# Performance work log

Hardware: AMD Instinct MI355X
Metric: run time of the kernel (lower is better)

## Reference

```python
import jax, jax.numpy as jnp
import numpy as np


def _lstm_dir(x, w_ih, w_hh, b_ih, b_hh, reverse):
    # x: [B, L, D]; w_ih: [4H, D]; w_hh: [4H, H]; PyTorch gate order i,f,g,o
    B = x.shape[0]
    H = w_hh.shape[1]
    h0 = jnp.zeros((B, H), x.dtype)

    def cell(carry, x_t):
        h, c = carry
        z = x_t @ w_ih.T + h @ w_hh.T + b_ih + b_hh
        i, f, g, o = jnp.split(z, 4, axis=-1)
        c = jax.nn.sigmoid(f) * c + jax.nn.sigmoid(i) * jnp.tanh(g)
        h = jax.nn.sigmoid(o) * jnp.tanh(c)
        return (h, c), h

    _, hs = jax.lax.scan(cell, (h0, h0), jnp.swapaxes(x, 0, 1), reverse=reverse)
    return jnp.swapaxes(hs, 0, 1)  # [B, L, H]


def setup_inputs() -> dict:
    key = jax.random.key(0)
    ks = jax.random.split(key, 16)
    B, L, V, D, H, E, A = 32, 128, 30000, 300, 128, 34, 36
    s = 0.05
    rn = lambda k, shape: jax.random.normal(k, shape, jnp.float32) * s
    return {
        "input_ids": jax.random.randint(ks[0], (B, L), 0, V),
        "emb": rn(ks[1], (V, D)),
        "w_ih_f": rn(ks[2], (4 * H, D)), "w_hh_f": rn(ks[3], (4 * H, H)),
        "b_ih_f": rn(ks[4], (4 * H,)), "b_hh_f": rn(ks[5], (4 * H,)),
        "w_ih_b": rn(ks[6], (4 * H, D)), "w_hh_b": rn(ks[7], (4 * H, H)),
        "b_ih_b": rn(ks[8], (4 * H,)), "b_hh_b": rn(ks[9], (4 * H,)),
        "event_w": rn(ks[10], (E, 2 * H)), "event_b": rn(ks[11], (E,)),
        "arg_w": rn(ks[12], (A, 4 * H + E - 1)), "arg_b": rn(ks[13], (A,)),
    }


def reference(input_ids, emb, w_ih_f, w_hh_f, b_ih_f, b_hh_f,
              w_ih_b, w_hh_b, b_ih_b, b_hh_b,
              event_w, event_b, arg_w, arg_b):
    # Eval mode: dropout is identity. No labels -> return (event_logits, arguments_logits).
    B, L = input_ids.shape
    E = event_b.shape[0]
    x = emb[input_ids]  # [B, L, D]
    h_f = _lstm_dir(x, w_ih_f, w_hh_f, b_ih_f, b_hh_f, False)
    h_b = _lstm_dir(x, w_ih_b, w_hh_b, b_ih_b, b_hh_b, True)
    hidden = jnp.concatenate([h_f, h_b], axis=-1)  # [B, L, 2H]
    col_range = jnp.arange(E - 1)
    g0 = jnp.zeros((B, L, E - 1), hidden.dtype)  # running g_trg_arg memory

    def step(g, h_i):  # h_i: [B, 2H] = trigger hidden state at timestep i
        ev_logit = h_i @ event_w.T + event_b  # [B, E]
        ev_pred = jnp.argmax(ev_logit, axis=-1)  # [B]
        trig = jnp.broadcast_to(h_i[:, None, :], hidden.shape)  # [B, L, 2H]
        ah = jnp.concatenate([hidden, trig, g], axis=-1)  # [B, L, 4H+E-1]
        arg_logit = ah @ arg_w.T + arg_b  # [B, L, A]
        arg_pred = jnp.argmax(arg_logit, axis=-1)  # [B, L]
        # Vectorized update_g_trg_arg: for batch items with ev_pred>0, set
        # column (ev_pred-1) to 1 wherever arg_pred>0, else keep previous value.
        mask_ev = ev_pred > 0  # [B]
        col = jnp.where(mask_ev, ev_pred - 1, 0)  # [B]
        onehot = (col[:, None] == col_range[None, :]) & mask_ev[:, None]  # [B, E-1]
        cond = onehot[:, None, :] & (arg_pred[:, :, None] > 0)  # [B, L, E-1]
        g = jnp.where(cond, jnp.ones((), g.dtype), g)
        return g, (ev_logit, arg_logit)

    _, (ev_logits, arg_logits) = jax.lax.scan(step, g0, jnp.swapaxes(hidden, 0, 1))
    event_logits = jnp.swapaxes(ev_logits, 0, 1)  # [B, L, E]
    arguments_logits = jnp.swapaxes(arg_logits, 0, 1)  # [B, L, L, A]
    return event_logits, arguments_logits
```

## Files before the change

kernel.cpp:

```cpp
#include <hip/hip_runtime.h>
#include <hip/hip_bf16.h>
#include <stdint.h>

#define B_  32
#define L_  128
#define D_  300
#define DP_ 304
#define H_  128
#define G_  512
#define E_  34
#define A_  36
#define M_  4096
#define NC_ 106
#define NCP 112
#define CH_ 8
#define NCH 16
#define LCH 8
#define NCHK (L_ / LCH)

__device__ __forceinline__ float sigf(float x){ return 1.0f / (1.0f + expf(-x)); }

__global__ void k_prep1(const float* __restrict__ wihf, const float* __restrict__ wihb,
                        float* __restrict__ WT){
    int k = blockIdx.x;
    int d = blockIdx.y;
    int n = threadIdx.x;
    const float* w = d ? wihb : wihf;
    WT[((size_t)d * DP_ + k) * G_ + n] = (k < D_) ? w[(size_t)n * D_ + k] : 0.0f;
}

__global__ void k_prep2(const float* __restrict__ evw, const float* __restrict__ evb,
                        const float* __restrict__ argw, const float* __restrict__ argb,
                        float* __restrict__ WcatT, float* __restrict__ biasv){
    int k = blockIdx.x;
    int n = threadIdx.x;
    if (n >= NCP) return;
    float v = 0.0f;
    if (n < E_)       v = evw[(size_t)n * 256 + k];
    else if (n < 70)  v = argw[(size_t)(n - 34) * 545 + k];
    else if (n < NC_) v = argw[(size_t)(n - 70) * 545 + 256 + k];
    WcatT[(size_t)k * NCP + n] = v;
    if (k == 0){
        float bv = 0.0f;
        if (n < E_) bv = evb[n];
        else if (n < 70) bv = argb[n - 34];
        biasv[n] = bv;
    }
}

__launch_bounds__(256)
__global__ void k_gemm1(const int* __restrict__ ids, const float* __restrict__ emb,
                        const float* __restrict__ WT,
                        const float* __restrict__ bihf, const float* __restrict__ bhhf,
                        const float* __restrict__ bihb, const float* __restrict__ bhhb,
                        float* __restrict__ XW){
    __shared__ __align__(16) float xs[DP_][8];
    int d  = blockIdx.y;
    int m0 = blockIdx.x * 8;
    int tid = threadIdx.x;
    for (int idx = tid; idx < 8 * DP_; idx += 256){
        int r = idx / DP_, k = idx % DP_;
        int id = ids[m0 + r];
        xs[k][r] = (k < D_) ? emb[(size_t)id * D_ + k] : 0.0f;
    }
    __syncthreads();
    int n0 = tid, n1 = tid + 256;
    const float* w0 = WT + (size_t)d * DP_ * G_ + n0;
    const float* w1 = WT + (size_t)d * DP_ * G_ + n1;
    const float4* xs4 = (const float4*)xs;
    float acc0[8] = {}, acc1[8] = {};
    #pragma unroll 2
    for (int k = 0; k < D_; k++){
        float wv0 = w0[(size_t)k * G_];
        float wv1 = w1[(size_t)k * G_];
        float4 xA = xs4[k * 2], xB = xs4[k * 2 + 1];
        acc0[0] += xA.x * wv0; acc0[1] += xA.y * wv0;
        acc0[2] += xA.z * wv0; acc0[3] += xA.w * wv0;
        acc0[4] += xB.x * wv0; acc0[5] += xB.y * wv0;
        acc0[6] += xB.z * wv0; acc0[7] += xB.w * wv0;
        acc1[0] += xA.x * wv1; acc1[1] += xA.y * wv1;
        acc1[2] += xA.z * wv1; acc1[3] += xA.w * wv1;
        acc1[4] += xB.x * wv1; acc1[5] += xB.y * wv1;
        acc1[6] += xB.z * wv1; acc1[7] += xB.w * wv1;
    }
    float bias0 = d ? (bihb[n0] + bhhb[n0]) : (bihf[n0] + bhhf[n0]);
    float bias1 = d ? (bihb[n1] + bhhb[n1]) : (bihf[n1] + bhhf[n1]);
    for (int r = 0; r < 8; r++){
        XW[((size_t)d * M_ + m0 + r) * G_ + n0] = acc0[r] + bias0;
        XW[((size_t)d * M_ + m0 + r) * G_ + n1] = acc1[r] + bias1;
    }
}

#define PF(XR, CHI)                                                             \
{                                                                               \
    if ((CHI) < NCHK){                                                          \
        _Pragma("unroll")                                                       \
        for (int j = 0; j < LCH; j++){                                          \
            int s_ = (CHI) * LCH + j;                                           \
            int t_ = d ? (L_ - 1 - s_) : s_;                                    \
            XR[j] = xwn[(size_t)t_ * G_];                                       \
        }                                                                       \
    }                                                                           \
}

#define STEP8(XR, CHI)                                                          \
{                                                                               \
    _Pragma("unroll")                                                           \
    for (int j = 0; j < LCH; j++){                                              \
        int s_ = (CHI) * LCH + j;                                               \
        const float4* hc = (const float4*)((j & 1) ? hb1 : hb0);                \
        float a0=0.f,a1=0.f,a2=0.f,a3=0.f;                                      \
        _Pragma("unroll")                                                       \
        for (int q = 0; q < 32; q++){                                           \
            float4 hv = hc[q];                                                  \
            a0 += wv[q].x * hv.x; a1 += wv[q].y * hv.y;                         \
            a2 += wv[q].z * hv.z; a3 += wv[q].w * hv.w;                         \
        }                                                                       \
        float z = XR[j] + ((a0 + a1) + (a2 + a3));                              \
        float v = (gi == 2) ? tanhf(z) : sigf(z);                               \
        float Fv = __shfl_xor(v, 16);                                           \
        float Gv = __shfl_xor(v, 32);                                           \
        float Ov = __shfl_xor(v, 48);                                           \
        if (lane < 16){                                                         \
            c = Fv * c + v * Gv;                                                \
            float h = Ov * tanhf(c);                                            \
            float* hw = (j & 1) ? hb0 : hb1;                                    \
            hw[n16] = h;                                                        \
            hist[(size_t)(s_) * H_ + n16] = h;                                  \
        }                                                                       \
        __syncthreads();                                                        \
    }                                                                           \
}

__launch_bounds__(512, 2)
__global__ void k_lstm(const float* __restrict__ XW, const float* __restrict__ whhf,
                       const float* __restrict__ whhb, float* __restrict__ Hid){
    __shared__ __align__(16) float hb0[H_];
    __shared__ __align__(16) float hb1[H_];
    __shared__ __align__(16) float hist[L_ * H_];
    int bid = blockIdx.x;
    int d = bid >> 5, b = bid & 31;
    int tid = threadIdx.x;
    int wvi  = tid >> 6;
    int lane = tid & 63;
    int n16  = wvi * 16 + (lane & 15);
    int gi   = lane >> 4;
    int row  = gi * H_ + n16;
    const float* whh = d ? whhb : whhf;
    const float4* wr = (const float4*)(whh + (size_t)row * H_);
    float4 wv[32];
    #pragma unroll
    for (int q = 0; q < 32; q++) wv[q] = wr[q];
    float c = 0.0f;
    if (tid < H_) hb0[tid] = 0.0f;
    __syncthreads();
    const float* xwn = XW + ((size_t)d * M_ + (size_t)b * L_) * G_ + row;
    float xA[LCH], xB[LCH];
    PF(xA, 0)
    #pragma unroll 1
    for (int cp = 0; cp < NCHK / 2; cp++){
        PF(xB, 2 * cp + 1)
        STEP8(xA, 2 * cp)
        PF(xA, 2 * cp + 2)
        STEP8(xB, 2 * cp + 1)
    }
    const float4* hist4 = (const float4*)hist;
    #pragma unroll
    for (int q = 0; q < 8; q++){
        int idx = tid + q * 512;
        int sl = idx >> 5, n4 = idx & 31;
        int t_ = d ? (L_ - 1 - sl) : sl;
        *(float4*)(Hid + ((size_t)b * L_ + t_) * 256 + d * H_ + n4 * 4) =
            hist4[(size_t)sl * 32 + n4];
    }
}

__launch_bounds__(128)
__global__ void k_heads2(const float* __restrict__ Hid, const float* __restrict__ WcatT,
                         const float* __restrict__ biasv,
                         float* __restrict__ out0, float* __restrict__ Base,
                         float* __restrict__ T2, int* __restrict__ Evcol){
    __shared__ float hs[256];
    __shared__ float evl[E_];
    int m = blockIdx.x;
    int tid = threadIdx.x;
    hs[tid]       = Hid[(size_t)m * 256 + tid];
    hs[tid + 128] = Hid[(size_t)m * 256 + 128 + tid];
    __syncthreads();
    float acc = 0.0f;
    if (tid < NC_){
        const float* wc = WcatT + tid;
        for (int k = 0; k < 256; k++) acc += hs[k] * wc[(size_t)k * NCP];
        acc += biasv[tid];
    }
    if (tid < E_){
        out0[(size_t)m * E_ + tid] = acc;
        evl[tid] = acc;
    } else if (tid < 70){
        Base[(size_t)m * A_ + (tid - 34)] = acc;
    } else if (tid < NC_){
        T2[(size_t)m * A_ + (tid - 70)] = acc;
    }
    __syncthreads();
    if (tid == 0){
        float best = evl[0]; int bi = 0;
        for (int e = 1; e < E_; e++){
            float v = evl[e];
            if (v > best){ best = v; bi = e; }
        }
        Evcol[m] = bi - 1;
    }
}

__launch_bounds__(128)
__global__ void k_scan1(const float* __restrict__ Base, const float* __restrict__ T2,
                        const int* __restrict__ Evcol, const float* __restrict__ argw,
                        float* __restrict__ Snap, uint64_t* __restrict__ MaskSnap){
    __shared__ float t2s[L_ * A_];
    __shared__ float wgs[33 * A_];
    __shared__ int   evc[L_];
    int b = blockIdx.x;
    int l = threadIdx.x;
    for (int idx = l; idx < L_ * A_; idx += 128)
        t2s[idx] = T2[(size_t)b * L_ * A_ + idx];
    for (int idx = l; idx < 33 * A_; idx += 128){
        int c = idx / A_, a = idx % A_;
        wgs[idx] = argw[(size_t)a * 545 + 512 + c];
    }
    evc[l] = Evcol[b * L_ + l];
    __syncthreads();
    float bg[A_];
    {
        const float* bp = Base + ((size_t)b * L_ + l) * A_;
        #pragma unroll
        for (int a = 0; a < A_; a++) bg[a] = bp[a];
    }
    uint64_t mask = 0;
    #pragma unroll 1
    for (int i = 0; i < L_; i++){
        if ((i & (CH_ - 1)) == 0){
            int ch = i >> 3;
            float* sp = Snap + (((size_t)b * NCH + ch) * L_ + l) * A_;
            #pragma unroll
            for (int a = 0; a < A_; a++) sp[a] = bg[a];
            MaskSnap[((size_t)b * NCH + ch) * L_ + l] = mask;
        }
        const float* tr = t2s + i * A_;
        float lg0 = bg[0] + tr[0];
        float m1  = bg[1] + tr[1];
        #pragma unroll
        for (int a = 2; a < A_; a++) m1 = fmaxf(m1, bg[a] + tr[a]);
        bool apos = m1 > lg0;
        int cc = evc[i];
        if (cc >= 0 && apos && !((mask >> cc) & 1ull)){
            mask |= 1ull << cc;
            const float* wc = wgs + cc * A_;
            #pragma unroll
            for (int a = 0; a < A_; a++) bg[a] += wc[a];
        }
    }
}

__launch_bounds__(128)
__global__ void k_scan2(const float* __restrict__ T2, const int* __restrict__ Evcol,
                        const float* __restrict__ argw,
                        const float* __restrict__ Snap, const uint64_t* __restrict__ MaskSnap,
                        float* __restrict__ argout){
    __shared__ float t2s[CH_ * A_];
    __shared__ float wgs[33 * A_];
    __shared__ int   evc[CH_];
    int ch = blockIdx.x;
    int b  = blockIdx.y;
    int l  = threadIdx.x;
    int i0 = ch * CH_;
    for (int idx = l; idx < CH_ * A_; idx += 128)
        t2s[idx] = T2[((size_t)b * L_ + i0) * A_ + idx];
    for (int idx = l; idx < 33 * A_; idx += 128){
        int c = idx / A_, a = idx % A_;
        wgs[idx] = argw[(size_t)a * 545 + 512 + c];
    }
    if (l < CH_) evc[l] = Evcol[b * L_ + i0 + l];
    __syncthreads();
    float bg[A_];
    {
        const float* sp = Snap + (((size_t)b * NCH + ch) * L_ + l) * A_;
        #pragma unroll
        for (int a = 0; a < A_; a++) bg[a] = sp[a];
    }
    uint64_t mask = MaskSnap[((size_t)b * NCH + ch) * L_ + l];
    #pragma unroll 1
    for (int s = 0; s < CH_; s++){
        int i = i0 + s;
        const float* tr = t2s + s * A_;
        float lg[A_];
        #pragma unroll
        for (int a = 0; a < A_; a++) lg[a] = bg[a] + tr[a];
        float m1 = lg[1];
        #pragma unroll
        for (int a = 2; a < A_; a++) m1 = fmaxf(m1, lg[a]);
        bool apos = m1 > lg[0];
        float* op = argout + (((size_t)b * L_ + i) * L_ + l) * A_;
        #pragma unroll
        for (int q = 0; q < 9; q++){
            float4 v; v.x = lg[4*q]; v.y = lg[4*q+1]; v.z = lg[4*q+2]; v.w = lg[4*q+3];
            *(float4*)(op + 4 * q) = v;
        }
        int cc = evc[s];
        if (cc >= 0 && apos && !((mask >> cc) & 1ull)){
            mask |= 1ull << cc;
            const float* wc = wgs + cc * A_;
            #pragma unroll
            for (int a = 0; a < A_; a++) bg[a] += wc[a];
        }
    }
}

extern "C" void kernel_launch(void* const* d_in, const int* in_sizes, int n_in,
                              void* d_out, int out_size, void* d_ws, size_t ws_size,
                              hipStream_t stream){
    const int*   ids  = (const int*)  d_in[0];
    const float* emb  = (const float*)d_in[1];
    const float* wihf = (const float*)d_in[2];
    const float* whhf = (const float*)d_in[3];
    const float* bihf = (const float*)d_in[4];
    const float* bhhf = (const float*)d_in[5];
    const float* wihb = (const float*)d_in[6];
    const float* whhb = (const float*)d_in[7];
    const float* bihb = (const float*)d_in[8];
    const float* bhhb = (const float*)d_in[9];
    const float* evw  = (const float*)d_in[10];
    const float* evb  = (const float*)d_in[11];
    const float* argw = (const float*)d_in[12];
    const float* argb = (const float*)d_in[13];

    float* out0   = (float*)d_out;
    float* argout = out0 + (size_t)M_ * E_;

    char* w = (char*)d_ws;
    float* WT    = (float*)w; w += (size_t)2 * DP_ * G_ * 4;
    float* XW    = (float*)w; w += (size_t)2 * M_ * G_ * 4;
    float* Hid   = (float*)w; w += (size_t)M_ * 256 * 4;
    float* WcatT = (float*)w; w += (size_t)256 * NCP * 4;
    float* biasv = (float*)w; w += (size_t)NCP * 4;
    float* Base  = (float*)w; w += (size_t)M_ * A_ * 4;
    float* T2    = (float*)w; w += (size_t)M_ * A_ * 4;
    int*   Evcol = (int*)w;   w += (size_t)M_ * 4;

    float*    Snap     = XW;
    uint64_t* MaskSnap = (uint64_t*)(XW + (size_t)B_ * NCH * L_ * A_);

    k_prep1<<<dim3(DP_, 2), 512, 0, stream>>>(wihf, wihb, WT);
    k_prep2<<<256, 128, 0, stream>>>(evw, evb, argw, argb, WcatT, biasv);
    k_gemm1<<<dim3(M_ / 8, 2), 256, 0, stream>>>(ids, emb, WT, bihf, bhhf, bihb, bhhb, XW);
    k_lstm<<<64, 512, 0, stream>>>(XW, whhf, whhb, Hid);
    k_heads2<<<M_, 128, 0, stream>>>(Hid, WcatT, biasv, out0, Base, T2, Evcol);
    k_scan1<<<B_, 128, 0, stream>>>(Base, T2, Evcol, argw, Snap, MaskSnap);
    k_scan2<<<dim3(NCH, B_), 128, 0, stream>>>(T2, Evcol, argw, Snap, MaskSnap, argout);
}
```

Before: 392.4 us.

## Use packed FMA in LSTM and input GEMM, widen GEMM row tile, share gates via LDS

The input-projection GEMM now processes 16 rows per block instead of 8, caches token ids in shared memory, and accumulates with 2-wide packed float FMAs. The LSTM recurrence switches to packed FMA over weight pairs. Thread-to-gate mapping becomes one thread per gate row, and gate values are exchanged through a shared-memory buffer with an extra barrier instead of wave shuffles. The aim is to roughly halve FMA issue count on the serial recurrence and improve weight reuse in the GEMM, at the cost of one more __syncthreads per timestep and more accumulator registers.

```diff
diff --git a/kernel.cpp b/kernel.cpp
--- a/kernel.cpp
+++ b/kernel.cpp
@@ -17,6 +17,9 @@
 #define NCH 16
 #define LCH 8
 #define NCHK (L_ / LCH)
+#define BM_ 16
+
+typedef float f2 __attribute__((ext_vector_type(2)));
 
 __device__ __forceinline__ float sigf(float x){ return 1.0f / (1.0f + expf(-x)); }
 
@@ -54,40 +57,46 @@
                         const float* __restrict__ bihf, const float* __restrict__ bhhf,
                         const float* __restrict__ bihb, const float* __restrict__ bhhb,
                         float* __restrict__ XW){
-    __shared__ __align__(16) float xs[DP_][8];
+    __shared__ __align__(16) float xs[DP_][BM_];
+    __shared__ int ids_s[BM_];
     int d  = blockIdx.y;
-    int m0 = blockIdx.x * 8;
+    int m0 = blockIdx.x * BM_;
     int tid = threadIdx.x;
-    for (int idx = tid; idx < 8 * DP_; idx += 256){
-        int r = idx / DP_, k = idx % DP_;
-        int id = ids[m0 + r];
-        xs[k][r] = (k < D_) ? emb[(size_t)id * D_ + k] : 0.0f;
+    if (tid < BM_) ids_s[tid] = ids[m0 + tid];
+    __syncthreads();
+    for (int idx = tid; idx < BM_ * DP_; idx += 256){
+        int k = idx >> 4, r = idx & (BM_ - 1);
+        xs[k][r] = (k < D_) ? emb[(size_t)ids_s[r] * D_ + k] : 0.0f;
     }
     __syncthreads();
     int n0 = tid, n1 = tid + 256;
     const float* w0 = WT + (size_t)d * DP_ * G_ + n0;
     const float* w1 = WT + (size_t)d * DP_ * G_ + n1;
     const float4* xs4 = (const float4*)xs;
-    float acc0[8] = {}, acc1[8] = {};
+    f2 acc0[8] = {}, acc1[8] = {};
     #pragma unroll 2
     for (int k = 0; k < D_; k++){
         float wv0 = w0[(size_t)k * G_];
         float wv1 = w1[(size_t)k * G_];
-        float4 xA = xs4[k * 2], xB = xs4[k * 2 + 1];
-        acc0[0] += xA.x * wv0; acc0[1] += xA.y * wv0;
-        acc0[2] += xA.z * wv0; acc0[3] += xA.w * wv0;
-        acc0[4] += xB.x * wv0; acc0[5] += xB.y * wv0;
-        acc0[6] += xB.z * wv0; acc0[7] += xB.w * wv0;
-        acc1[0] += xA.x * wv1; acc1[1] += xA.y * wv1;
-        acc1[2] += xA.z * wv1; acc1[3] += xA.w * wv1;
-        acc1[4] += xB.x * wv1; acc1[5] += xB.y * wv1;
-        acc1[6] += xB.z * wv1; acc1[7] += xB.w * wv1;
+        f2 wb0 = {wv0, wv0}, wb1 = {wv1, wv1};
+        #pragma unroll
+        for (int rq = 0; rq < 4; rq++){
+            float4 x = xs4[k * 4 + rq];
+            f2 xlo = {x.x, x.y}, xhi = {x.z, x.w};
+            acc0[2*rq]   = __builtin_elementwise_fma(wb0, xlo, acc0[2*rq]);
+            acc0[2*rq+1] = __builtin_elementwise_fma(wb0, xhi, acc0[2*rq+1]);
+            acc1[2*rq]   = __builtin_elementwise_fma(wb1, xlo, acc1[2*rq]);
+            acc1[2*rq+1] = __builtin_elementwise_fma(wb1, xhi, acc1[2*rq+1]);
+        }
     }
     float bias0 = d ? (bihb[n0] + bhhb[n0]) : (bihf[n0] + bhhf[n0]);
     float bias1 = d ? (bihb[n1] + bhhb[n1]) : (bihf[n1] + bhhf[n1]);
-    for (int r = 0; r < 8; r++){
-        XW[((size_t)d * M_ + m0 + r) * G_ + n0] = acc0[r] + bias0;
-        XW[((size_t)d * M_ + m0 + r) * G_ + n1] = acc1[r] + bias1;
+    #pragma unroll
+    for (int r = 0; r < BM_; r++){
+        float v0 = (r & 1) ? acc0[r >> 1].y : acc0[r >> 1].x;
+        float v1 = (r & 1) ? acc1[r >> 1].y : acc1[r >> 1].x;
+        XW[((size_t)d * M_ + m0 + r) * G_ + n0] = v0 + bias0;
+        XW[((size_t)d * M_ + m0 + r) * G_ + n1] = v1 + bias1;
     }
 }
 
@@ -108,25 +117,25 @@
     _Pragma("unroll")                                                           \
     for (int j = 0; j < LCH; j++){                                              \
         int s_ = (CHI) * LCH + j;                                               \
-        const float4* hc = (const float4*)((j & 1) ? hb1 : hb0);                \
-        float a0=0.f,a1=0.f,a2=0.f,a3=0.f;                                      \
+        f2 a01 = {0.f, 0.f}, a23 = {0.f, 0.f};                                  \
+        const float4* hc = (const float4*)hbuf;                                 \
         _Pragma("unroll")                                                       \
         for (int q = 0; q < 32; q++){                                           \
             float4 hv = hc[q];                                                  \
-            a0 += wv[q].x * hv.x; a1 += wv[q].y * hv.y;                         \
-            a2 += wv[q].z * hv.z; a3 += wv[q].w * hv.w;                         \
+            f2 h01 = {hv.x, hv.y}, h23 = {hv.z, hv.w};                          \
+            a01 = __builtin_elementwise_fma(wp[2*q],   h01, a01);               \
+            a23 = __builtin_elementwise_fma(wp[2*q+1], h23, a23);               \
         }                                                                       \
-        float z = XR[j] + ((a0 + a1) + (a2 + a3));                              \
-        float v = (gi == 2) ? tanhf(z) : sigf(z);                               \
-        float Fv = __shfl_xor(v, 16);                                           \
-        float Gv = __shfl_xor(v, 32);                                           \
-        float Ov = __shfl_xor(v, 48);                                           \
-        if (lane < 16){                                                         \
-            c = Fv * c + v * Gv;                                                \
-            float h = Ov * tanhf(c);                                            \
-            float* hw = (j & 1) ? hb0 : hb1;                                    \
-            hw[n16] = h;                                                        \
-            hist[(size_t)(s_) * H_ + n16] = h;                                  \
+        float z = XR[j] + ((a01.x + a01.y) + (a23.x + a23.y));                  \
+        float v = gate_g ? tanhf(z) : sigf(z);                                  \
+        zbuf[n] = v;                                                            \
+        __syncthreads();                                                        \
+        if (n < H_){                                                            \
+            float F = zbuf[H_ + n], G = zbuf[2*H_ + n], O = zbuf[3*H_ + n];     \
+            c = F * c + v * G;                                                  \
+            float h = O * tanhf(c);                                             \
+            hbuf[n] = h;                                                        \
+            hist[(size_t)(s_) * H_ + n] = h;                                    \
         }                                                                       \
         __syncthreads();                                                        \
     }                                                                           \
@@ -135,26 +144,22 @@
 __launch_bounds__(512, 2)
 __global__ void k_lstm(const float* __restrict__ XW, const float* __restrict__ whhf,
                        const float* __restrict__ whhb, float* __restrict__ Hid){
-    __shared__ __align__(16) float hb0[H_];
-    __shared__ __align__(16) float hb1[H_];
+    __shared__ __align__(16) float hbuf[H_];
+    __shared__ float zbuf[G_];
     __shared__ __align__(16) float hist[L_ * H_];
     int bid = blockIdx.x;
     int d = bid >> 5, b = bid & 31;
-    int tid = threadIdx.x;
-    int wvi  = tid >> 6;
-    int lane = tid & 63;
-    int n16  = wvi * 16 + (lane & 15);
-    int gi   = lane >> 4;
-    int row  = gi * H_ + n16;
+    int n = threadIdx.x;
+    bool gate_g = ((n >> 7) == 2);
     const float* whh = d ? whhb : whhf;
-    const float4* wr = (const float4*)(whh + (size_t)row * H_);
-    float4 wv[32];
+    const f2* wr2 = (const f2*)(whh + (size_t)n * H_);
+    f2 wp[64];
     #pragma unroll
-    for (int q = 0; q < 32; q++) wv[q] = wr[q];
+    for (int q = 0; q < 64; q++) wp[q] = wr2[q];
     float c = 0.0f;
-    if (tid < H_) hb0[tid] = 0.0f;
-    __syncthreads();
-    const float* xwn = XW + ((size_t)d * M_ + (size_t)b * L_) * G_ + row;
+    if (n < H_) hbuf[n] = 0.0f;
+    __syncthreads();
+    const float* xwn = XW + ((size_t)d * M_ + (size_t)b * L_) * G_ + n;
     float xA[LCH], xB[LCH];
     PF(xA, 0)
     #pragma unroll 1
@@ -167,7 +172,7 @@
     const float4* hist4 = (const float4*)hist;
     #pragma unroll
     for (int q = 0; q < 8; q++){
-        int idx = tid + q * 512;
+        int idx = n + q * 512;
         int sl = idx >> 5, n4 = idx & 31;
         int t_ = d ? (L_ - 1 - sl) : sl;
         *(float4*)(Hid + ((size_t)b * L_ + t_) * 256 + d * H_ + n4 * 4) =
@@ -351,7 +356,7 @@
 
     k_prep1<<<dim3(DP_, 2), 512, 0, stream>>>(wihf, wihb, WT);
     k_prep2<<<256, 128, 0, stream>>>(evw, evb, argw, argb, WcatT, biasv);
-    k_gemm1<<<dim3(M_ / 8, 2), 256, 0, stream>>>(ids, emb, WT, bihf, bhhf, bihb, bhhb, XW);
+    k_gemm1<<<dim3(M_ / BM_, 2), 256, 0, stream>>>(ids, emb, WT, bihf, bhhf, bihb, bhhb, XW);
     k_lstm<<<64, 512, 0, stream>>>(XW, whhf, whhb, Hid);
     k_heads2<<<M_, 128, 0, stream>>>(Hid, WcatT, biasv, out0, Base, T2, Evcol);
     k_scan1<<<B_, 128, 0, stream>>>(Base, T2, Evcol, argw, Snap, MaskSnap);
```

After: 388.8 us. About the same (-0.9%).
